# Optimization experiments

Measured on AMD Instinct MI355X. Metric: run time of the kernel, lower is better.

Reference implementation:

```python
import jax, jax.numpy as jnp
import numpy as np

D = 1024      # hidden_size
F = 4096      # intermediate_size
E = 16        # num_experts
TOPK = 2      # num_experts_per_tok
B, L = 1, 2048


def setup_inputs() -> dict:
    key = jax.random.key(0)
    ks = jax.random.split(key, 5)
    s = 0.02
    return {
        "x": jax.random.normal(ks[0], (B, L, D), dtype=jnp.float32),
        "gate_w": jax.random.normal(ks[1], (E, D), dtype=jnp.float32) * s,
        "w1s": jax.random.normal(ks[2], (E, F, D), dtype=jnp.float32) * s,  # per-expert w1 (out,in)
        "w2s": jax.random.normal(ks[3], (E, D, F), dtype=jnp.float32) * s,  # per-expert w2
        "w3s": jax.random.normal(ks[4], (E, F, D), dtype=jnp.float32) * s,  # per-expert w3
    }


def reference(x, gate_w, w1s, w2s, w3s):
    b, l, d = x.shape
    xf = x.reshape(-1, d)                                   # [T, D]
    router_logits = xf @ gate_w.T                           # [T, E]
    topw, topi = jax.lax.top_k(router_logits.astype(jnp.float32), TOPK)
    topw = jax.nn.softmax(topw, axis=-1).astype(x.dtype)    # [T, K]
    T = xf.shape[0]
    # dense combine weights: zero for unselected experts (same math as masked loop)
    combine = jnp.zeros((T, E), x.dtype).at[jnp.arange(T)[:, None], topi].add(topw)

    def body(acc, ew):
        w1, w2, w3, cw = ew                                 # cw: [T]
        h = jax.nn.silu(xf @ w1.T) * (xf @ w3.T)            # [T, F]
        return acc + cw[:, None] * (h @ w2.T), None

    out, _ = jax.lax.scan(body, jnp.zeros_like(xf), (w1s, w2s, w3s, combine.T))
    return out.reshape(b, l, d), router_logits
```

## Files before the change

kernel.cpp:

```cpp
#include <hip/hip_runtime.h>

#define D_DIM 1024
#define F_DIM 4096
#define E_NUM 16
#define T_NUM 2048

typedef __bf16 bf16x8 __attribute__((ext_vector_type(8)));
typedef float f32x4 __attribute__((ext_vector_type(4)));

__device__ __forceinline__ unsigned pack2bf(float a, float b) {
  unsigned ua = __builtin_bit_cast(unsigned, a);
  unsigned ub = __builtin_bit_cast(unsigned, b);
  return ((ub + 0x8000u) & 0xffff0000u) | ((ua + 0x8000u) >> 16);
}
__device__ __forceinline__ unsigned short f2bf(float a) {
  unsigned ua = __builtin_bit_cast(unsigned, a);
  return (unsigned short)((ua + 0x8000u) >> 16);
}
__device__ __forceinline__ bf16x8 cvt8(f32x4 a, f32x4 b) {
  bf16x8 r;
  r[0] = (__bf16)a[0]; r[1] = (__bf16)a[1]; r[2] = (__bf16)a[2]; r[3] = (__bf16)a[3];
  r[4] = (__bf16)b[0]; r[5] = (__bf16)b[1]; r[6] = (__bf16)b[2]; r[7] = (__bf16)b[3];
  return r;
}
__device__ __forceinline__ void gload16(const void* g, void* l) {
  __builtin_amdgcn_global_load_lds(
      (const __attribute__((address_space(1))) unsigned*)g,
      (__attribute__((address_space(3))) unsigned*)l, 16, 0, 0);
}

__global__ __launch_bounds__(256) void moe_xcast(
    const float* __restrict__ x, unsigned short* __restrict__ xbf)
{
  int i = blockIdx.x * 256 + threadIdx.x;
  const f32x4* p = (const f32x4*)x + (size_t)i * 2;
  f32x4 a = p[0], b = p[1];
  uint4 o;
  o.x = pack2bf(a[0], a[1]); o.y = pack2bf(a[2], a[3]);
  o.z = pack2bf(b[0], b[1]); o.w = pack2bf(b[2], b[3]);
  ((uint4*)xbf)[i] = o;
}

__global__ __launch_bounds__(256) void moe_router(
    const float* __restrict__ x, const float* __restrict__ gate,
    float* __restrict__ logits_out, int* __restrict__ topi, float* __restrict__ topw)
{
  __shared__ float lg[16][17];
  int tid = threadIdx.x;
  int tbase = blockIdx.x * 16;
  int tt = tid >> 4, e = tid & 15;
  const float4* xr = (const float4*)(x + (size_t)(tbase + tt) * D_DIM);
  const float4* gw = (const float4*)(gate + (size_t)e * D_DIM);
  float acc = 0.f;
  #pragma unroll 4
  for (int k = 0; k < D_DIM / 4; ++k) {
    float4 a = xr[k], b = gw[k];
    acc += a.x * b.x + a.y * b.y + a.z * b.z + a.w * b.w;
  }
  lg[tt][e] = acc;
  logits_out[(size_t)(tbase + tt) * E_NUM + e] = acc;
  __syncthreads();
  if (tid < 16) {
    int t = tid;
    float best = -1e30f; int i0 = 0;
    #pragma unroll
    for (int j = 0; j < 16; ++j) { float v = lg[t][j]; if (v > best) { best = v; i0 = j; } }
    float best1 = -1e30f; int i1 = 0;
    #pragma unroll
    for (int j = 0; j < 16; ++j) { if (j == i0) continue; float v = lg[t][j]; if (v > best1) { best1 = v; i1 = j; } }
    float e1 = __expf(best1 - best);
    float inv = 1.f / (1.f + e1);
    int gt = tbase + t;
    topi[gt * 2]     = i0;  topi[gt * 2 + 1] = i1;
    topw[gt * 2]     = inv; topw[gt * 2 + 1] = e1 * inv;
  }
}

__global__ __launch_bounds__(1024) void moe_route_build(
    const int* __restrict__ topi,
    int* __restrict__ cnt, int* __restrict__ rowbase,
    int* __restrict__ rowlist, int* __restrict__ rowpos)
{
  __shared__ int scnt[16];
  __shared__ int sbase[17];
  int wave = threadIdx.x >> 6;
  int lane = threadIdx.x & 63;
  int total = 0;
  for (int c = 0; c < (T_NUM * 2) / 64; ++c) {
    int s = c * 64 + lane;
    unsigned long long m = __ballot(topi[s] == wave);
    total += __popcll(m);
  }
  if (lane == 0) scnt[wave] = total;
  __syncthreads();
  if (threadIdx.x == 0) {
    int acc = 0;
    for (int e2 = 0; e2 < 16; ++e2) { sbase[e2] = acc; cnt[e2] = scnt[e2]; acc += scnt[e2]; }
    sbase[16] = acc;
    for (int e2 = 0; e2 <= 16; ++e2) rowbase[e2] = sbase[e2];
  }
  __syncthreads();
  int running = sbase[wave];
  for (int c = 0; c < (T_NUM * 2) / 64; ++c) {
    int s = c * 64 + lane;
    int ei = topi[s];
    unsigned long long m = __ballot(ei == wave);
    if (ei == wave) {
      int pos = running + __popcll(m & ((1ull << lane) - 1ull));
      rowlist[pos] = s;
      rowpos[s] = pos;
    }
    running += __popcll(m);
  }
}

__global__ __launch_bounds__(256, 2) void moe_gemm1(
    const unsigned short* __restrict__ xbf, const float* __restrict__ w1s, const float* __restrict__ w3s,
    const int* __restrict__ cnt, const int* __restrict__ rowbase, const int* __restrict__ rowlist,
    unsigned short* __restrict__ H)
{
  int e = blockIdx.z, mt = blockIdx.y, nt = blockIdx.x;
  int Ne = cnt[e];
  if (mt * 128 >= Ne) return;
  int rbase = rowbase[e];

  __shared__ char smem[81920];

  int tid = threadIdx.x, lane = tid & 63, wave = tid >> 6;

  const char* px[2];
  #pragma unroll
  for (int it = 0; it < 2; ++it) {
    int r = (wave * 2 + it) * 16 + (lane >> 2);
    int lr = mt * 128 + r;
    int tok = (lr < Ne) ? (rowlist[rbase + lr] >> 1) : 0;
    int c = (lane & 3) ^ ((r >> 1) & 3);
    px[it] = (const char*)(xbf + (size_t)tok * D_DIM) + c * 16;
  }
  const float* w1e = w1s + (size_t)e * F_DIM * D_DIM + (size_t)(nt * 128) * D_DIM;
  const float* w3e = w3s + (size_t)e * F_DIM * D_DIM + (size_t)(nt * 128) * D_DIM;
  const char* p1[4]; const char* p3[4];
  #pragma unroll
  for (int it = 0; it < 4; ++it) {
    int r = (wave * 4 + it) * 8 + (lane >> 3);
    int c = (lane & 7) ^ (r & 7);
    p1[it] = (const char*)(w1e + (size_t)r * D_DIM) + c * 16;
    p3[it] = (const char*)(w3e + (size_t)r * D_DIM) + c * 16;
  }

  int wm = wave >> 1, wn = wave & 1;
  int lr16 = lane & 15, lq = lane >> 4;

  unsigned offA[4];
  #pragma unroll
  for (int mi = 0; mi < 4; ++mi) {
    int m = wm * 64 + mi * 16 + lr16;
    offA[mi] = (unsigned)(m * 64 + ((lq ^ ((m >> 1) & 3)) * 16));
  }
  unsigned offB[4][2];
  #pragma unroll
  for (int ni = 0; ni < 4; ++ni) {
    int n = wn * 64 + ni * 16 + lr16;
    #pragma unroll
    for (int h = 0; h < 2; ++h)
      offB[ni][h] = (unsigned)(n * 128 + (((lq * 2 + h) ^ (n & 7)) * 16));
  }

  f32x4 acc1[4][4], acc3[4][4];
  #pragma unroll
  for (int i = 0; i < 4; ++i)
    #pragma unroll
    for (int j = 0; j < 4; ++j) { acc1[i][j] = {0.f,0.f,0.f,0.f}; acc3[i][j] = {0.f,0.f,0.f,0.f}; }

  unsigned xdst = (unsigned)((wave * 2) * 1024 + lane * 16);
  unsigned wdst = (unsigned)((wave * 4) * 1024 + lane * 16);

  auto STAGE = [&](unsigned bsel, int ks) {
    gload16(px[0] + ks * 64, smem + bsel * 8192 + xdst);
    gload16(px[1] + ks * 64, smem + bsel * 8192 + xdst + 1024);
    #pragma unroll
    for (int it = 0; it < 4; ++it) {
      gload16(p1[it] + ks * 128, smem + 16384 + bsel * 16384 + wdst + it * 1024);
      gload16(p3[it] + ks * 128, smem + 49152 + bsel * 16384 + wdst + it * 1024);
    }
  };

  STAGE(0, 0);
  unsigned buf = 0;
  for (int ks = 0; ks < 32; ++ks) {
    if (ks < 31) {
      STAGE(buf ^ 1u, ks + 1);
      asm volatile("s_waitcnt vmcnt(10)" ::: "memory");
    } else {
      asm volatile("s_waitcnt vmcnt(0)" ::: "memory");
    }
    __builtin_amdgcn_s_barrier();
    unsigned xb = buf * 8192;
    unsigned w1b = 16384 + buf * 16384;
    unsigned w3b = 49152 + buf * 16384;
    bf16x8 af[4], b1f[4], b3f[4];
    #pragma unroll
    for (int mi = 0; mi < 4; ++mi)
      af[mi] = *(const bf16x8*)(smem + xb + offA[mi]);
    #pragma unroll
    for (int ni = 0; ni < 4; ++ni) {
      b1f[ni] = cvt8(*(const f32x4*)(smem + w1b + offB[ni][0]),
                     *(const f32x4*)(smem + w1b + offB[ni][1]));
      b3f[ni] = cvt8(*(const f32x4*)(smem + w3b + offB[ni][0]),
                     *(const f32x4*)(smem + w3b + offB[ni][1]));
    }
    #pragma unroll
    for (int ni = 0; ni < 4; ++ni)
      #pragma unroll
      for (int mi = 0; mi < 4; ++mi) {
        acc1[mi][ni] = __builtin_amdgcn_mfma_f32_16x16x32_bf16(af[mi], b1f[ni], acc1[mi][ni], 0, 0, 0);
        acc3[mi][ni] = __builtin_amdgcn_mfma_f32_16x16x32_bf16(af[mi], b3f[ni], acc3[mi][ni], 0, 0, 0);
      }
    __builtin_amdgcn_s_barrier();
    buf ^= 1u;
  }

  #pragma unroll
  for (int mi = 0; mi < 4; ++mi) {
    int mb = wm * 64 + mi * 16 + lq * 4;
    #pragma unroll
    for (int r = 0; r < 4; ++r) {
      int lrow = mt * 128 + mb + r;
      if (lrow < Ne) {
        size_t hrow = (size_t)(rbase + lrow) * F_DIM;
        #pragma unroll
        for (int ni = 0; ni < 4; ++ni) {
          int f = nt * 128 + wn * 64 + ni * 16 + lr16;
          float a1v = acc1[mi][ni][r];
          float a3v = acc3[mi][ni][r];
          float hv = (a1v / (1.f + __expf(-a1v))) * a3v;
          H[hrow + f] = f2bf(hv);
        }
      }
    }
  }
}

__global__ __launch_bounds__(256, 2) void moe_gemm2(
    const unsigned short* __restrict__ H, const float* __restrict__ w2s,
    const int* __restrict__ cnt, const int* __restrict__ rowbase,
    unsigned short* __restrict__ Ybf)
{
  int e = blockIdx.z, mt = blockIdx.y, nt = blockIdx.x;
  int Ne = cnt[e];
  if (mt * 128 >= Ne) return;
  int rbase = rowbase[e];

  __shared__ char smem[65536];

  int tid = threadIdx.x, lane = tid & 63, wave = tid >> 6;

  const char* pa[4];
  #pragma unroll
  for (int it = 0; it < 4; ++it) {
    int r = (wave * 4 + it) * 8 + (lane >> 3);
    int c = (lane & 7) ^ (r & 7);
    int grow = mt * 128 + r; if (grow >= Ne) grow = Ne - 1;
    pa[it] = (const char*)(H + (size_t)(rbase + grow) * F_DIM) + c * 16;
  }
  const float* w2e = w2s + (size_t)e * D_DIM * F_DIM + (size_t)(nt * 64) * F_DIM;
  const char* pb[4];
  #pragma unroll
  for (int it = 0; it < 4; ++it) {
    int r = (wave * 4 + it) * 4 + (lane >> 4);
    int c = (lane & 15) ^ (r & 7);
    pb[it] = (const char*)(w2e + (size_t)r * F_DIM) + c * 16;
  }

  int wm = wave >> 1, wn = wave & 1;
  int lr16 = lane & 15, lq = lane >> 4;

  f32x4 acc[4][2];
  #pragma unroll
  for (int i = 0; i < 4; ++i) { acc[i][0] = {0.f,0.f,0.f,0.f}; acc[i][1] = {0.f,0.f,0.f,0.f}; }

  unsigned dst = (unsigned)((wave * 4) * 1024 + lane * 16);

  auto STAGE = [&](unsigned bsel, int ks) {
    #pragma unroll
    for (int it = 0; it < 4; ++it) {
      gload16(pa[it] + ks * 128, smem + bsel * 16384 + dst + it * 1024);
      gload16(pb[it] + ks * 256, smem + 32768 + bsel * 16384 + dst + it * 1024);
    }
  };

  STAGE(0, 0);
  unsigned buf = 0;
  for (int ks = 0; ks < 64; ++ks) {
    if (ks < 63) {
      STAGE(buf ^ 1u, ks + 1);
      asm volatile("s_waitcnt vmcnt(8)" ::: "memory");
    } else {
      asm volatile("s_waitcnt vmcnt(0)" ::: "memory");
    }
    __builtin_amdgcn_s_barrier();
    unsigned ab = buf * 16384;
    unsigned bb = 32768 + buf * 16384;
    #pragma unroll
    for (int ksub = 0; ksub < 2; ++ksub) {
      bf16x8 af[4], bf[2];
      #pragma unroll
      for (int mi = 0; mi < 4; ++mi) {
        int m = wm * 64 + mi * 16 + lr16;
        unsigned off = (unsigned)(m * 128 + (((ksub * 4 + lq) ^ (m & 7)) * 16));
        af[mi] = *(const bf16x8*)(smem + ab + off);
      }
      #pragma unroll
      for (int ni = 0; ni < 2; ++ni) {
        int n = wn * 32 + ni * 16 + lr16;
        unsigned o0 = (unsigned)(n * 256 + (((ksub * 8 + lq * 2 + 0) ^ (n & 7)) * 16));
        unsigned o1 = (unsigned)(n * 256 + (((ksub * 8 + lq * 2 + 1) ^ (n & 7)) * 16));
        bf[ni] = cvt8(*(const f32x4*)(smem + bb + o0), *(const f32x4*)(smem + bb + o1));
      }
      #pragma unroll
      for (int mi = 0; mi < 4; ++mi)
        #pragma unroll
        for (int ni = 0; ni < 2; ++ni)
          acc[mi][ni] = __builtin_amdgcn_mfma_f32_16x16x32_bf16(af[mi], bf[ni], acc[mi][ni], 0, 0, 0);
    }
    __builtin_amdgcn_s_barrier();
    buf ^= 1u;
  }

  #pragma unroll
  for (int mi = 0; mi < 4; ++mi) {
    int mb = wm * 64 + mi * 16 + lq * 4;
    #pragma unroll
    for (int r = 0; r < 4; ++r) {
      int lrow = mt * 128 + mb + r;
      if (lrow < Ne) {
        size_t yrow = (size_t)(rbase + lrow) * D_DIM;
        #pragma unroll
        for (int ni = 0; ni < 2; ++ni) {
          int d = nt * 64 + wn * 32 + ni * 16 + lr16;
          Ybf[yrow + d] = f2bf(acc[mi][ni][r]);
        }
      }
    }
  }
}

__global__ __launch_bounds__(128) void moe_combine(
    const unsigned short* __restrict__ Ybf, const int* __restrict__ rowpos,
    const float* __restrict__ topw, float* __restrict__ out)
{
  int t = blockIdx.x, tid = threadIdx.x;
  int r0 = rowpos[t * 2], r1 = rowpos[t * 2 + 1];
  float p0 = topw[t * 2], p1 = topw[t * 2 + 1];
  uint4 a = ((const uint4*)(Ybf + (size_t)r0 * D_DIM))[tid];
  uint4 b = ((const uint4*)(Ybf + (size_t)r1 * D_DIM))[tid];
  float4 o0, o1;
  #define LO(u) __builtin_bit_cast(float, (unsigned)((u) << 16))
  #define HI(u) __builtin_bit_cast(float, (unsigned)((u) & 0xffff0000u))
  o0.x = p0 * LO(a.x) + p1 * LO(b.x);  o0.y = p0 * HI(a.x) + p1 * HI(b.x);
  o0.z = p0 * LO(a.y) + p1 * LO(b.y);  o0.w = p0 * HI(a.y) + p1 * HI(b.y);
  o1.x = p0 * LO(a.z) + p1 * LO(b.z);  o1.y = p0 * HI(a.z) + p1 * HI(b.z);
  o1.z = p0 * LO(a.w) + p1 * LO(b.w);  o1.w = p0 * HI(a.w) + p1 * HI(b.w);
  #undef LO
  #undef HI
  float4* orow = (float4*)(out + (size_t)t * D_DIM);
  orow[tid * 2]     = o0;
  orow[tid * 2 + 1] = o1;
}

extern "C" void kernel_launch(void* const* d_in, const int* in_sizes, int n_in,
                              void* d_out, int out_size, void* d_ws, size_t ws_size,
                              hipStream_t stream) {
  const float* x    = (const float*)d_in[0];
  const float* gate = (const float*)d_in[1];
  const float* w1   = (const float*)d_in[2];
  const float* w2   = (const float*)d_in[3];
  const float* w3   = (const float*)d_in[4];
  float* out    = (float*)d_out;
  float* logits = out + (size_t)T_NUM * D_DIM;

  char* ws = (char*)d_ws;
  int*   cnt     = (int*)(ws + 0);
  int*   rowbase = (int*)(ws + 64);
  int*   topi    = (int*)(ws + 1024);
  float* topw    = (float*)(ws + 1024 + 16384);
  int*   rowlist = (int*)(ws + 1024 + 32768);
  int*   rowpos  = (int*)(ws + 1024 + 49152);
  unsigned short* H   = (unsigned short*)(ws + 131072);
  unsigned short* Ybf = (unsigned short*)(ws + 131072 + 33554432);
  unsigned short* xbf = (unsigned short*)(ws + 131072 + 33554432 + 8388608);

  moe_xcast<<<(T_NUM * D_DIM) / (256 * 8), 256, 0, stream>>>(x, xbf);
  moe_router<<<T_NUM / 16, 256, 0, stream>>>(x, gate, logits, topi, topw);
  moe_route_build<<<1, 1024, 0, stream>>>(topi, cnt, rowbase, rowlist, rowpos);
  moe_gemm1<<<dim3(F_DIM / 128, T_NUM / 128, E_NUM), 256, 0, stream>>>(xbf, w1, w3, cnt, rowbase, rowlist, H);
  moe_gemm2<<<dim3(D_DIM / 64, T_NUM / 128, E_NUM), 256, 0, stream>>>(H, w2, cnt, rowbase, Ybf);
  moe_combine<<<T_NUM, 128, 0, stream>>>(Ybf, rowpos, topw, out);
}
```

Measured before the change: 365.7 us.

## Use 8 waves per block in both MoE GEMMs, halving per-wave tile

Both expert GEMM kernels move from 256 to 512 threads per block. Each wave now computes a narrower N slice (2 subtiles in gemm1, 1 in gemm2), and the global-to-LDS staging work and vmcnt thresholds are split to match. The aim is more waves per CU to hide memory and LDS latency, at the cost of less register-level reuse of A fragments per wave and more LDS reads per MFMA. The launch bound of 4 blocks per CU may not be reachable given the 80KB/64KB LDS per block.

```diff
diff --git a/kernel.cpp b/kernel.cpp
--- a/kernel.cpp
+++ b/kernel.cpp
@@ -114,7 +114,7 @@
   }
 }
 
-__global__ __launch_bounds__(256, 2) void moe_gemm1(
+__global__ __launch_bounds__(512, 4) void moe_gemm1(
     const unsigned short* __restrict__ xbf, const float* __restrict__ w1s, const float* __restrict__ w3s,
     const int* __restrict__ cnt, const int* __restrict__ rowbase, const int* __restrict__ rowlist,
     unsigned short* __restrict__ H)
@@ -128,27 +128,26 @@
 
   int tid = threadIdx.x, lane = tid & 63, wave = tid >> 6;
 
-  const char* px[2];
-  #pragma unroll
-  for (int it = 0; it < 2; ++it) {
-    int r = (wave * 2 + it) * 16 + (lane >> 2);
-    int lr = mt * 128 + r;
-    int tok = (lr < Ne) ? (rowlist[rbase + lr] >> 1) : 0;
-    int c = (lane & 3) ^ ((r >> 1) & 3);
-    px[it] = (const char*)(xbf + (size_t)tok * D_DIM) + c * 16;
-  }
+  int xr = wave * 16 + (lane >> 2);
+  {
+  }
+  int xlr = mt * 128 + xr;
+  int xtok = (xlr < Ne) ? (rowlist[rbase + xlr] >> 1) : 0;
+  int xc = (lane & 3) ^ ((xr >> 1) & 3);
+  const char* px = (const char*)(xbf + (size_t)xtok * D_DIM) + xc * 16;
+
   const float* w1e = w1s + (size_t)e * F_DIM * D_DIM + (size_t)(nt * 128) * D_DIM;
   const float* w3e = w3s + (size_t)e * F_DIM * D_DIM + (size_t)(nt * 128) * D_DIM;
-  const char* p1[4]; const char* p3[4];
-  #pragma unroll
-  for (int it = 0; it < 4; ++it) {
-    int r = (wave * 4 + it) * 8 + (lane >> 3);
+  const char* p1[2]; const char* p3[2];
+  #pragma unroll
+  for (int it = 0; it < 2; ++it) {
+    int r = (wave * 2 + it) * 8 + (lane >> 3);
     int c = (lane & 7) ^ (r & 7);
     p1[it] = (const char*)(w1e + (size_t)r * D_DIM) + c * 16;
     p3[it] = (const char*)(w3e + (size_t)r * D_DIM) + c * 16;
   }
 
-  int wm = wave >> 1, wn = wave & 1;
+  int wm = wave >> 2, wn = wave & 3;
   int lr16 = lane & 15, lq = lane >> 4;
 
   unsigned offA[4];
@@ -157,29 +156,28 @@
     int m = wm * 64 + mi * 16 + lr16;
     offA[mi] = (unsigned)(m * 64 + ((lq ^ ((m >> 1) & 3)) * 16));
   }
-  unsigned offB[4][2];
-  #pragma unroll
-  for (int ni = 0; ni < 4; ++ni) {
-    int n = wn * 64 + ni * 16 + lr16;
+  unsigned offB[2][2];
+  #pragma unroll
+  for (int ni = 0; ni < 2; ++ni) {
+    int n = wn * 32 + ni * 16 + lr16;
     #pragma unroll
     for (int h = 0; h < 2; ++h)
       offB[ni][h] = (unsigned)(n * 128 + (((lq * 2 + h) ^ (n & 7)) * 16));
   }
 
-  f32x4 acc1[4][4], acc3[4][4];
+  f32x4 acc1[4][2], acc3[4][2];
   #pragma unroll
   for (int i = 0; i < 4; ++i)
     #pragma unroll
-    for (int j = 0; j < 4; ++j) { acc1[i][j] = {0.f,0.f,0.f,0.f}; acc3[i][j] = {0.f,0.f,0.f,0.f}; }
-
-  unsigned xdst = (unsigned)((wave * 2) * 1024 + lane * 16);
-  unsigned wdst = (unsigned)((wave * 4) * 1024 + lane * 16);
+    for (int j = 0; j < 2; ++j) { acc1[i][j] = {0.f,0.f,0.f,0.f}; acc3[i][j] = {0.f,0.f,0.f,0.f}; }
+
+  unsigned xdst = (unsigned)(wave * 1024 + lane * 16);
+  unsigned wdst = (unsigned)((wave * 2) * 1024 + lane * 16);
 
   auto STAGE = [&](unsigned bsel, int ks) {
-    gload16(px[0] + ks * 64, smem + bsel * 8192 + xdst);
-    gload16(px[1] + ks * 64, smem + bsel * 8192 + xdst + 1024);
-    #pragma unroll
-    for (int it = 0; it < 4; ++it) {
+    gload16(px + ks * 64, smem + bsel * 8192 + xdst);
+    #pragma unroll
+    for (int it = 0; it < 2; ++it) {
       gload16(p1[it] + ks * 128, smem + 16384 + bsel * 16384 + wdst + it * 1024);
       gload16(p3[it] + ks * 128, smem + 49152 + bsel * 16384 + wdst + it * 1024);
     }
@@ -190,7 +188,7 @@
   for (int ks = 0; ks < 32; ++ks) {
     if (ks < 31) {
       STAGE(buf ^ 1u, ks + 1);
-      asm volatile("s_waitcnt vmcnt(10)" ::: "memory");
+      asm volatile("s_waitcnt vmcnt(5)" ::: "memory");
     } else {
       asm volatile("s_waitcnt vmcnt(0)" ::: "memory");
     }
@@ -198,24 +196,22 @@
     unsigned xb = buf * 8192;
     unsigned w1b = 16384 + buf * 16384;
     unsigned w3b = 49152 + buf * 16384;
-    bf16x8 af[4], b1f[4], b3f[4];
+    bf16x8 af[4];
     #pragma unroll
     for (int mi = 0; mi < 4; ++mi)
       af[mi] = *(const bf16x8*)(smem + xb + offA[mi]);
     #pragma unroll
-    for (int ni = 0; ni < 4; ++ni) {
-      b1f[ni] = cvt8(*(const f32x4*)(smem + w1b + offB[ni][0]),
-                     *(const f32x4*)(smem + w1b + offB[ni][1]));
-      b3f[ni] = cvt8(*(const f32x4*)(smem + w3b + offB[ni][0]),
-                     *(const f32x4*)(smem + w3b + offB[ni][1]));
-    }
-    #pragma unroll
-    for (int ni = 0; ni < 4; ++ni)
+    for (int ni = 0; ni < 2; ++ni) {
+      bf16x8 b1 = cvt8(*(const f32x4*)(smem + w1b + offB[ni][0]),
+                       *(const f32x4*)(smem + w1b + offB[ni][1]));
+      bf16x8 b3 = cvt8(*(const f32x4*)(smem + w3b + offB[ni][0]),
+                       *(const f32x4*)(smem + w3b + offB[ni][1]));
       #pragma unroll
       for (int mi = 0; mi < 4; ++mi) {
-        acc1[mi][ni] = __builtin_amdgcn_mfma_f32_16x16x32_bf16(af[mi], b1f[ni], acc1[mi][ni], 0, 0, 0);
-        acc3[mi][ni] = __builtin_amdgcn_mfma_f32_16x16x32_bf16(af[mi], b3f[ni], acc3[mi][ni], 0, 0, 0);
-      }
+        acc1[mi][ni] = __builtin_amdgcn_mfma_f32_16x16x32_bf16(af[mi], b1, acc1[mi][ni], 0, 0, 0);
+        acc3[mi][ni] = __builtin_amdgcn_mfma_f32_16x16x32_bf16(af[mi], b3, acc3[mi][ni], 0, 0, 0);
+      }
+    }
     __builtin_amdgcn_s_barrier();
     buf ^= 1u;
   }
@@ -229,8 +225,8 @@
       if (lrow < Ne) {
         size_t hrow = (size_t)(rbase + lrow) * F_DIM;
         #pragma unroll
-        for (int ni = 0; ni < 4; ++ni) {
-          int f = nt * 128 + wn * 64 + ni * 16 + lr16;
+        for (int ni = 0; ni < 2; ++ni) {
+          int f = nt * 128 + wn * 32 + ni * 16 + lr16;
           float a1v = acc1[mi][ni][r];
           float a3v = acc3[mi][ni][r];
           float hv = (a1v / (1.f + __expf(-a1v))) * a3v;
@@ -241,7 +237,7 @@
   }
 }
 
-__global__ __launch_bounds__(256, 2) void moe_gemm2(
+__global__ __launch_bounds__(512, 4) void moe_gemm2(
     const unsigned short* __restrict__ H, const float* __restrict__ w2s,
     const int* __restrict__ cnt, const int* __restrict__ rowbase,
     unsigned short* __restrict__ Ybf)
@@ -255,35 +251,35 @@
 
   int tid = threadIdx.x, lane = tid & 63, wave = tid >> 6;
 
-  const char* pa[4];
-  #pragma unroll
-  for (int it = 0; it < 4; ++it) {
-    int r = (wave * 4 + it) * 8 + (lane >> 3);
+  const char* pa[2];
+  #pragma unroll
+  for (int it = 0; it < 2; ++it) {
+    int r = (wave * 2 + it) * 8 + (lane >> 3);
     int c = (lane & 7) ^ (r & 7);
     int grow = mt * 128 + r; if (grow >= Ne) grow = Ne - 1;
     pa[it] = (const char*)(H + (size_t)(rbase + grow) * F_DIM) + c * 16;
   }
   const float* w2e = w2s + (size_t)e * D_DIM * F_DIM + (size_t)(nt * 64) * F_DIM;
-  const char* pb[4];
-  #pragma unroll
-  for (int it = 0; it < 4; ++it) {
-    int r = (wave * 4 + it) * 4 + (lane >> 4);
+  const char* pb[2];
+  #pragma unroll
+  for (int it = 0; it < 2; ++it) {
+    int r = (wave * 2 + it) * 4 + (lane >> 4);
     int c = (lane & 15) ^ (r & 7);
     pb[it] = (const char*)(w2e + (size_t)r * F_DIM) + c * 16;
   }
 
-  int wm = wave >> 1, wn = wave & 1;
+  int wm = wave >> 2, wn = wave & 3;
   int lr16 = lane & 15, lq = lane >> 4;
 
-  f32x4 acc[4][2];
-  #pragma unroll
-  for (int i = 0; i < 4; ++i) { acc[i][0] = {0.f,0.f,0.f,0.f}; acc[i][1] = {0.f,0.f,0.f,0.f}; }
-
-  unsigned dst = (unsigned)((wave * 4) * 1024 + lane * 16);
+  f32x4 acc[4];
+  #pragma unroll
+  for (int i = 0; i < 4; ++i) acc[i] = {0.f,0.f,0.f,0.f};
+
+  unsigned dst = (unsigned)((wave * 2) * 1024 + lane * 16);
 
   auto STAGE = [&](unsigned bsel, int ks) {
     #pragma unroll
-    for (int it = 0; it < 4; ++it) {
+    for (int it = 0; it < 2; ++it) {
       gload16(pa[it] + ks * 128, smem + bsel * 16384 + dst + it * 1024);
       gload16(pb[it] + ks * 256, smem + 32768 + bsel * 16384 + dst + it * 1024);
     }
@@ -294,34 +290,29 @@
   for (int ks = 0; ks < 64; ++ks) {
     if (ks < 63) {
       STAGE(buf ^ 1u, ks + 1);
-      asm volatile("s_waitcnt vmcnt(8)" ::: "memory");
+      asm volatile("s_waitcnt vmcnt(4)" ::: "memory");
     } else {
       asm volatile("s_waitcnt vmcnt(0)" ::: "memory");
     }
     __builtin_amdgcn_s_barrier();
     unsigned ab = buf * 16384;
     unsigned bb = 32768 + buf * 16384;
+    int n = wn * 16 + lr16;
     #pragma unroll
     for (int ksub = 0; ksub < 2; ++ksub) {
-      bf16x8 af[4], bf[2];
+      bf16x8 bf;
+      {
+        unsigned o0 = (unsigned)(n * 256 + (((ksub * 8 + lq * 2 + 0) ^ (n & 7)) * 16));
+        unsigned o1 = (unsigned)(n * 256 + (((ksub * 8 + lq * 2 + 1) ^ (n & 7)) * 16));
+        bf = cvt8(*(const f32x4*)(smem + bb + o0), *(const f32x4*)(smem + bb + o1));
+      }
       #pragma unroll
       for (int mi = 0; mi < 4; ++mi) {
         int m = wm * 64 + mi * 16 + lr16;
         unsigned off = (unsigned)(m * 128 + (((ksub * 4 + lq) ^ (m & 7)) * 16));
-        af[mi] = *(const bf16x8*)(smem + ab + off);
-      }
-      #pragma unroll
-      for (int ni = 0; ni < 2; ++ni) {
-        int n = wn * 32 + ni * 16 + lr16;
-        unsigned o0 = (unsigned)(n * 256 + (((ksub * 8 + lq * 2 + 0) ^ (n & 7)) * 16));
-        unsigned o1 = (unsigned)(n * 256 + (((ksub * 8 + lq * 2 + 1) ^ (n & 7)) * 16));
-        bf[ni] = cvt8(*(const f32x4*)(smem + bb + o0), *(const f32x4*)(smem + bb + o1));
-      }
-      #pragma unroll
-      for (int mi = 0; mi < 4; ++mi)
-        #pragma unroll
-        for (int ni = 0; ni < 2; ++ni)
-          acc[mi][ni] = __builtin_amdgcn_mfma_f32_16x16x32_bf16(af[mi], bf[ni], acc[mi][ni], 0, 0, 0);
+        bf16x8 af = *(const bf16x8*)(smem + ab + off);
+        acc[mi] = __builtin_amdgcn_mfma_f32_16x16x32_bf16(af, bf, acc[mi], 0, 0, 0);
+      }
     }
     __builtin_amdgcn_s_barrier();
     buf ^= 1u;
@@ -335,11 +326,8 @@
       int lrow = mt * 128 + mb + r;
       if (lrow < Ne) {
         size_t yrow = (size_t)(rbase + lrow) * D_DIM;
-        #pragma unroll
-        for (int ni = 0; ni < 2; ++ni) {
-          int d = nt * 64 + wn * 32 + ni * 16 + lr16;
-          Ybf[yrow + d] = f2bf(acc[mi][ni][r]);
-        }
+        int d = nt * 64 + wn * 16 + lr16;
+        Ybf[yrow + d] = f2bf(acc[mi][r]);
       }
     }
   }
@@ -393,7 +381,7 @@
   moe_xcast<<<(T_NUM * D_DIM) / (256 * 8), 256, 0, stream>>>(x, xbf);
   moe_router<<<T_NUM / 16, 256, 0, stream>>>(x, gate, logits, topi, topw);
   moe_route_build<<<1, 1024, 0, stream>>>(topi, cnt, rowbase, rowlist, rowpos);
-  moe_gemm1<<<dim3(F_DIM / 128, T_NUM / 128, E_NUM), 256, 0, stream>>>(xbf, w1, w3, cnt, rowbase, rowlist, H);
-  moe_gemm2<<<dim3(D_DIM / 64, T_NUM / 128, E_NUM), 256, 0, stream>>>(H, w2, cnt, rowbase, Ybf);
+  moe_gemm1<<<dim3(F_DIM / 128, T_NUM / 128, E_NUM), 512, 0, stream>>>(xbf, w1, w3, cnt, rowbase, rowlist, H);
+  moe_gemm2<<<dim3(D_DIM / 64, T_NUM / 128, E_NUM), 512, 0, stream>>>(H, w2, cnt, rowbase, Ybf);
   moe_combine<<<T_NUM, 128, 0, stream>>>(Ybf, rowpos, topw, out);
 }
```

After: 370.2 us. No clear change (+1.2%).

## Make MoE GEMMs persistent per expert/N-tile with 256-row tiles and XCD mapping

Applied to the files above, without the earlier changes.

Both expert GEMMs now launch one 512-thread block per (expert, N-tile) and loop over 256-row M tiles inside the block, instead of launching a 3D grid of 128-row tiles. Block IDs are mapped so that each expert's blocks land on the same XCD, which should let the fp32 weight tiles be shared in that XCD's L2. Doubling the M tile to 256 rows cuts how many times the large fp32 weights are streamed from memory, since a typical expert now fits in one tile. The cost is possible load imbalance across experts with different token counts, and fewer independent blocks to hide latency.

```diff
diff --git a/kernel.cpp b/kernel.cpp
--- a/kernel.cpp
+++ b/kernel.cpp
@@ -114,40 +114,41 @@
   }
 }
 
-__global__ __launch_bounds__(256, 2) void moe_gemm1(
+__global__ __launch_bounds__(512, 2) void moe_gemm1(
     const unsigned short* __restrict__ xbf, const float* __restrict__ w1s, const float* __restrict__ w3s,
     const int* __restrict__ cnt, const int* __restrict__ rowbase, const int* __restrict__ rowlist,
     unsigned short* __restrict__ H)
 {
-  int e = blockIdx.z, mt = blockIdx.y, nt = blockIdx.x;
+  int bid = blockIdx.x;
+  int xcd = bid & 7, j = bid >> 3;
+  int e = xcd * 2 + (j >> 5);
+  int nt = j & 31;
   int Ne = cnt[e];
-  if (mt * 128 >= Ne) return;
   int rbase = rowbase[e];
-
-  __shared__ char smem[81920];
+  int nmt = (Ne + 255) >> 8;
+
+  __shared__ char smem[98304];
 
   int tid = threadIdx.x, lane = tid & 63, wave = tid >> 6;
 
-  const char* px[2];
-  #pragma unroll
-  for (int it = 0; it < 2; ++it) {
-    int r = (wave * 2 + it) * 16 + (lane >> 2);
-    int lr = mt * 128 + r;
-    int tok = (lr < Ne) ? (rowlist[rbase + lr] >> 1) : 0;
-    int c = (lane & 3) ^ ((r >> 1) & 3);
-    px[it] = (const char*)(xbf + (size_t)tok * D_DIM) + c * 16;
-  }
   const float* w1e = w1s + (size_t)e * F_DIM * D_DIM + (size_t)(nt * 128) * D_DIM;
   const float* w3e = w3s + (size_t)e * F_DIM * D_DIM + (size_t)(nt * 128) * D_DIM;
-  const char* p1[4]; const char* p3[4];
-  #pragma unroll
-  for (int it = 0; it < 4; ++it) {
-    int r = (wave * 4 + it) * 8 + (lane >> 3);
+  const char* p1[2]; const char* p3[2];
+  #pragma unroll
+  for (int it = 0; it < 2; ++it) {
+    int r = (wave * 2 + it) * 8 + (lane >> 3);
     int c = (lane & 7) ^ (r & 7);
     p1[it] = (const char*)(w1e + (size_t)r * D_DIM) + c * 16;
     p3[it] = (const char*)(w3e + (size_t)r * D_DIM) + c * 16;
   }
 
+  int xrr[2]; int xc[2];
+  #pragma unroll
+  for (int it = 0; it < 2; ++it) {
+    xrr[it] = (wave * 2 + it) * 16 + (lane >> 2);
+    xc[it] = (lane & 3) ^ ((xrr[it] >> 1) & 3);
+  }
+
   int wm = wave >> 1, wn = wave & 1;
   int lr16 = lane & 15, lq = lane >> 4;
 
@@ -166,179 +167,198 @@
       offB[ni][h] = (unsigned)(n * 128 + (((lq * 2 + h) ^ (n & 7)) * 16));
   }
 
-  f32x4 acc1[4][4], acc3[4][4];
-  #pragma unroll
-  for (int i = 0; i < 4; ++i)
-    #pragma unroll
-    for (int j = 0; j < 4; ++j) { acc1[i][j] = {0.f,0.f,0.f,0.f}; acc3[i][j] = {0.f,0.f,0.f,0.f}; }
-
   unsigned xdst = (unsigned)((wave * 2) * 1024 + lane * 16);
-  unsigned wdst = (unsigned)((wave * 4) * 1024 + lane * 16);
-
-  auto STAGE = [&](unsigned bsel, int ks) {
-    gload16(px[0] + ks * 64, smem + bsel * 8192 + xdst);
-    gload16(px[1] + ks * 64, smem + bsel * 8192 + xdst + 1024);
-    #pragma unroll
-    for (int it = 0; it < 4; ++it) {
-      gload16(p1[it] + ks * 128, smem + 16384 + bsel * 16384 + wdst + it * 1024);
-      gload16(p3[it] + ks * 128, smem + 49152 + bsel * 16384 + wdst + it * 1024);
-    }
-  };
-
-  STAGE(0, 0);
-  unsigned buf = 0;
-  for (int ks = 0; ks < 32; ++ks) {
-    if (ks < 31) {
-      STAGE(buf ^ 1u, ks + 1);
-      asm volatile("s_waitcnt vmcnt(10)" ::: "memory");
-    } else {
-      asm volatile("s_waitcnt vmcnt(0)" ::: "memory");
-    }
-    __builtin_amdgcn_s_barrier();
-    unsigned xb = buf * 8192;
-    unsigned w1b = 16384 + buf * 16384;
-    unsigned w3b = 49152 + buf * 16384;
-    bf16x8 af[4], b1f[4], b3f[4];
-    #pragma unroll
-    for (int mi = 0; mi < 4; ++mi)
-      af[mi] = *(const bf16x8*)(smem + xb + offA[mi]);
-    #pragma unroll
-    for (int ni = 0; ni < 4; ++ni) {
-      b1f[ni] = cvt8(*(const f32x4*)(smem + w1b + offB[ni][0]),
-                     *(const f32x4*)(smem + w1b + offB[ni][1]));
-      b3f[ni] = cvt8(*(const f32x4*)(smem + w3b + offB[ni][0]),
-                     *(const f32x4*)(smem + w3b + offB[ni][1]));
-    }
-    #pragma unroll
-    for (int ni = 0; ni < 4; ++ni)
-      #pragma unroll
-      for (int mi = 0; mi < 4; ++mi) {
-        acc1[mi][ni] = __builtin_amdgcn_mfma_f32_16x16x32_bf16(af[mi], b1f[ni], acc1[mi][ni], 0, 0, 0);
-        acc3[mi][ni] = __builtin_amdgcn_mfma_f32_16x16x32_bf16(af[mi], b3f[ni], acc3[mi][ni], 0, 0, 0);
-      }
-    __builtin_amdgcn_s_barrier();
-    buf ^= 1u;
-  }
-
-  #pragma unroll
-  for (int mi = 0; mi < 4; ++mi) {
-    int mb = wm * 64 + mi * 16 + lq * 4;
-    #pragma unroll
-    for (int r = 0; r < 4; ++r) {
-      int lrow = mt * 128 + mb + r;
-      if (lrow < Ne) {
-        size_t hrow = (size_t)(rbase + lrow) * F_DIM;
+  unsigned wdst = (unsigned)((wave * 2) * 1024 + lane * 16);
+
+  for (int mt = 0; mt < nmt; ++mt) {
+    const char* px[2];
+    #pragma unroll
+    for (int it = 0; it < 2; ++it) {
+      int xlr = mt * 256 + xrr[it];
+      int tok = (xlr < Ne) ? (rowlist[rbase + xlr] >> 1) : 0;
+      px[it] = (const char*)(xbf + (size_t)tok * D_DIM) + xc[it] * 16;
+    }
+
+    f32x4 acc1[4][4], acc3[4][4];
+    #pragma unroll
+    for (int i = 0; i < 4; ++i)
+      #pragma unroll
+      for (int jj = 0; jj < 4; ++jj) { acc1[i][jj] = {0.f,0.f,0.f,0.f}; acc3[i][jj] = {0.f,0.f,0.f,0.f}; }
+
+    auto STAGE = [&](unsigned bsel, int ks) {
+      gload16(px[0] + ks * 64, smem + bsel * 16384 + xdst);
+      gload16(px[1] + ks * 64, smem + bsel * 16384 + xdst + 1024);
+      #pragma unroll
+      for (int it = 0; it < 2; ++it) {
+        gload16(p1[it] + ks * 128, smem + 32768 + bsel * 16384 + wdst + it * 1024);
+        gload16(p3[it] + ks * 128, smem + 65536 + bsel * 16384 + wdst + it * 1024);
+      }
+    };
+
+    STAGE(0, 0);
+    unsigned buf = 0;
+    for (int ks = 0; ks < 32; ++ks) {
+      if (ks < 31) {
+        STAGE(buf ^ 1u, ks + 1);
+        asm volatile("s_waitcnt vmcnt(6)" ::: "memory");
+      } else {
+        asm volatile("s_waitcnt vmcnt(0)" ::: "memory");
+      }
+      __builtin_amdgcn_s_barrier();
+      unsigned xb = buf * 16384;
+      unsigned w1b = 32768 + buf * 16384;
+      unsigned w3b = 65536 + buf * 16384;
+      bf16x8 af[4];
+      #pragma unroll
+      for (int mi = 0; mi < 4; ++mi)
+        af[mi] = *(const bf16x8*)(smem + xb + offA[mi]);
+      #pragma unroll
+      for (int ni = 0; ni < 4; ++ni) {
+        bf16x8 b1 = cvt8(*(const f32x4*)(smem + w1b + offB[ni][0]),
+                         *(const f32x4*)(smem + w1b + offB[ni][1]));
+        bf16x8 b3 = cvt8(*(const f32x4*)(smem + w3b + offB[ni][0]),
+                         *(const f32x4*)(smem + w3b + offB[ni][1]));
         #pragma unroll
-        for (int ni = 0; ni < 4; ++ni) {
-          int f = nt * 128 + wn * 64 + ni * 16 + lr16;
-          float a1v = acc1[mi][ni][r];
-          float a3v = acc3[mi][ni][r];
-          float hv = (a1v / (1.f + __expf(-a1v))) * a3v;
-          H[hrow + f] = f2bf(hv);
+        for (int mi = 0; mi < 4; ++mi) {
+          acc1[mi][ni] = __builtin_amdgcn_mfma_f32_16x16x32_bf16(af[mi], b1, acc1[mi][ni], 0, 0, 0);
+          acc3[mi][ni] = __builtin_amdgcn_mfma_f32_16x16x32_bf16(af[mi], b3, acc3[mi][ni], 0, 0, 0);
         }
       }
-    }
-  }
-}
-
-__global__ __launch_bounds__(256, 2) void moe_gemm2(
+      __builtin_amdgcn_s_barrier();
+      buf ^= 1u;
+    }
+
+    #pragma unroll
+    for (int mi = 0; mi < 4; ++mi) {
+      int mb = wm * 64 + mi * 16 + lq * 4;
+      #pragma unroll
+      for (int r = 0; r < 4; ++r) {
+        int lrow = mt * 256 + mb + r;
+        if (lrow < Ne) {
+          size_t hrow = (size_t)(rbase + lrow) * F_DIM;
+          #pragma unroll
+          for (int ni = 0; ni < 4; ++ni) {
+            int f = nt * 128 + wn * 64 + ni * 16 + lr16;
+            float a1v = acc1[mi][ni][r];
+            float a3v = acc3[mi][ni][r];
+            float hv = (a1v / (1.f + __expf(-a1v))) * a3v;
+            H[hrow + f] = f2bf(hv);
+          }
+        }
+      }
+    }
+  }
+}
+
+__global__ __launch_bounds__(512, 2) void moe_gemm2(
     const unsigned short* __restrict__ H, const float* __restrict__ w2s,
     const int* __restrict__ cnt, const int* __restrict__ rowbase,
     unsigned short* __restrict__ Ybf)
 {
-  int e = blockIdx.z, mt = blockIdx.y, nt = blockIdx.x;
+  int bid = blockIdx.x;
+  int xcd = bid & 7, j = bid >> 3;
+  int e = xcd * 2 + (j >> 4);
+  int nt = j & 15;
   int Ne = cnt[e];
-  if (mt * 128 >= Ne) return;
   int rbase = rowbase[e];
-
-  __shared__ char smem[65536];
+  int nmt = (Ne + 255) >> 8;
+
+  __shared__ char smem[98304];
 
   int tid = threadIdx.x, lane = tid & 63, wave = tid >> 6;
 
-  const char* pa[4];
-  #pragma unroll
-  for (int it = 0; it < 4; ++it) {
-    int r = (wave * 4 + it) * 8 + (lane >> 3);
-    int c = (lane & 7) ^ (r & 7);
-    int grow = mt * 128 + r; if (grow >= Ne) grow = Ne - 1;
-    pa[it] = (const char*)(H + (size_t)(rbase + grow) * F_DIM) + c * 16;
-  }
   const float* w2e = w2s + (size_t)e * D_DIM * F_DIM + (size_t)(nt * 64) * F_DIM;
-  const char* pb[4];
-  #pragma unroll
-  for (int it = 0; it < 4; ++it) {
-    int r = (wave * 4 + it) * 4 + (lane >> 4);
+  const char* pb[2];
+  #pragma unroll
+  for (int it = 0; it < 2; ++it) {
+    int r = (wave * 2 + it) * 4 + (lane >> 4);
     int c = (lane & 15) ^ (r & 7);
     pb[it] = (const char*)(w2e + (size_t)r * F_DIM) + c * 16;
   }
 
+  int arr[4]; int ac[4];
+  #pragma unroll
+  for (int it = 0; it < 4; ++it) {
+    arr[it] = (wave * 4 + it) * 8 + (lane >> 3);
+    ac[it] = (lane & 7) ^ (arr[it] & 7);
+  }
+
   int wm = wave >> 1, wn = wave & 1;
   int lr16 = lane & 15, lq = lane >> 4;
 
-  f32x4 acc[4][2];
-  #pragma unroll
-  for (int i = 0; i < 4; ++i) { acc[i][0] = {0.f,0.f,0.f,0.f}; acc[i][1] = {0.f,0.f,0.f,0.f}; }
-
-  unsigned dst = (unsigned)((wave * 4) * 1024 + lane * 16);
-
-  auto STAGE = [&](unsigned bsel, int ks) {
+  unsigned dst2 = (unsigned)((wave * 2) * 1024 + lane * 16);
+  unsigned dst4 = (unsigned)((wave * 4) * 1024 + lane * 16);
+
+  for (int mt = 0; mt < nmt; ++mt) {
+    const char* pa[4];
     #pragma unroll
     for (int it = 0; it < 4; ++it) {
-      gload16(pa[it] + ks * 128, smem + bsel * 16384 + dst + it * 1024);
-      gload16(pb[it] + ks * 256, smem + 32768 + bsel * 16384 + dst + it * 1024);
-    }
-  };
-
-  STAGE(0, 0);
-  unsigned buf = 0;
-  for (int ks = 0; ks < 64; ++ks) {
-    if (ks < 63) {
-      STAGE(buf ^ 1u, ks + 1);
-      asm volatile("s_waitcnt vmcnt(8)" ::: "memory");
-    } else {
-      asm volatile("s_waitcnt vmcnt(0)" ::: "memory");
-    }
-    __builtin_amdgcn_s_barrier();
-    unsigned ab = buf * 16384;
-    unsigned bb = 32768 + buf * 16384;
-    #pragma unroll
-    for (int ksub = 0; ksub < 2; ++ksub) {
-      bf16x8 af[4], bf[2];
-      #pragma unroll
-      for (int mi = 0; mi < 4; ++mi) {
-        int m = wm * 64 + mi * 16 + lr16;
-        unsigned off = (unsigned)(m * 128 + (((ksub * 4 + lq) ^ (m & 7)) * 16));
-        af[mi] = *(const bf16x8*)(smem + ab + off);
-      }
-      #pragma unroll
-      for (int ni = 0; ni < 2; ++ni) {
-        int n = wn * 32 + ni * 16 + lr16;
-        unsigned o0 = (unsigned)(n * 256 + (((ksub * 8 + lq * 2 + 0) ^ (n & 7)) * 16));
-        unsigned o1 = (unsigned)(n * 256 + (((ksub * 8 + lq * 2 + 1) ^ (n & 7)) * 16));
-        bf[ni] = cvt8(*(const f32x4*)(smem + bb + o0), *(const f32x4*)(smem + bb + o1));
-      }
-      #pragma unroll
-      for (int mi = 0; mi < 4; ++mi)
-        #pragma unroll
-        for (int ni = 0; ni < 2; ++ni)
-          acc[mi][ni] = __builtin_amdgcn_mfma_f32_16x16x32_bf16(af[mi], bf[ni], acc[mi][ni], 0, 0, 0);
-    }
-    __builtin_amdgcn_s_barrier();
-    buf ^= 1u;
-  }
-
-  #pragma unroll
-  for (int mi = 0; mi < 4; ++mi) {
-    int mb = wm * 64 + mi * 16 + lq * 4;
-    #pragma unroll
-    for (int r = 0; r < 4; ++r) {
-      int lrow = mt * 128 + mb + r;
-      if (lrow < Ne) {
-        size_t yrow = (size_t)(rbase + lrow) * D_DIM;
+      int grow = mt * 256 + arr[it]; if (grow >= Ne) grow = Ne - 1;
+      pa[it] = (const char*)(H + (size_t)(rbase + grow) * F_DIM) + ac[it] * 16;
+    }
+
+    f32x4 acc[4][2];
+    #pragma unroll
+    for (int i = 0; i < 4; ++i) { acc[i][0] = {0.f,0.f,0.f,0.f}; acc[i][1] = {0.f,0.f,0.f,0.f}; }
+
+    auto STAGE = [&](unsigned bsel, int ks) {
+      #pragma unroll
+      for (int it = 0; it < 4; ++it)
+        gload16(pa[it] + ks * 128, smem + bsel * 32768 + dst4 + it * 1024);
+      #pragma unroll
+      for (int it = 0; it < 2; ++it)
+        gload16(pb[it] + ks * 256, smem + 65536 + bsel * 16384 + dst2 + it * 1024);
+    };
+
+    STAGE(0, 0);
+    unsigned buf = 0;
+    for (int ks = 0; ks < 64; ++ks) {
+      if (ks < 63) {
+        STAGE(buf ^ 1u, ks + 1);
+        asm volatile("s_waitcnt vmcnt(6)" ::: "memory");
+      } else {
+        asm volatile("s_waitcnt vmcnt(0)" ::: "memory");
+      }
+      __builtin_amdgcn_s_barrier();
+      unsigned ab = buf * 32768;
+      unsigned bb = 65536 + buf * 16384;
+      #pragma unroll
+      for (int ksub = 0; ksub < 2; ++ksub) {
+        bf16x8 bfr[2];
         #pragma unroll
         for (int ni = 0; ni < 2; ++ni) {
-          int d = nt * 64 + wn * 32 + ni * 16 + lr16;
-          Ybf[yrow + d] = f2bf(acc[mi][ni][r]);
+          int n = wn * 32 + ni * 16 + lr16;
+          unsigned o0 = (unsigned)(n * 256 + (((ksub * 8 + lq * 2 + 0) ^ (n & 7)) * 16));
+          unsigned o1 = (unsigned)(n * 256 + (((ksub * 8 + lq * 2 + 1) ^ (n & 7)) * 16));
+          bfr[ni] = cvt8(*(const f32x4*)(smem + bb + o0), *(const f32x4*)(smem + bb + o1));
+        }
+        #pragma unroll
+        for (int mi = 0; mi < 4; ++mi) {
+          int m = wm * 64 + mi * 16 + lr16;
+          unsigned off = (unsigned)(m * 128 + (((ksub * 4 + lq) ^ (m & 7)) * 16));
+          bf16x8 af = *(const bf16x8*)(smem + ab + off);
+          #pragma unroll
+          for (int ni = 0; ni < 2; ++ni)
+            acc[mi][ni] = __builtin_amdgcn_mfma_f32_16x16x32_bf16(af, bfr[ni], acc[mi][ni], 0, 0, 0);
+        }
+      }
+      __builtin_amdgcn_s_barrier();
+      buf ^= 1u;
+    }
+
+    #pragma unroll
+    for (int mi = 0; mi < 4; ++mi) {
+      int mb = wm * 64 + mi * 16 + lq * 4;
+      #pragma unroll
+      for (int r = 0; r < 4; ++r) {
+        int lrow = mt * 256 + mb + r;
+        if (lrow < Ne) {
+          size_t yrow = (size_t)(rbase + lrow) * D_DIM;
+          #pragma unroll
+          for (int ni = 0; ni < 2; ++ni) {
+            int d = nt * 64 + wn * 32 + ni * 16 + lr16;
+            Ybf[yrow + d] = f2bf(acc[mi][ni][r]);
+          }
         }
       }
     }
@@ -393,7 +413,7 @@
   moe_xcast<<<(T_NUM * D_DIM) / (256 * 8), 256, 0, stream>>>(x, xbf);
   moe_router<<<T_NUM / 16, 256, 0, stream>>>(x, gate, logits, topi, topw);
   moe_route_build<<<1, 1024, 0, stream>>>(topi, cnt, rowbase, rowlist, rowpos);
-  moe_gemm1<<<dim3(F_DIM / 128, T_NUM / 128, E_NUM), 256, 0, stream>>>(xbf, w1, w3, cnt, rowbase, rowlist, H);
-  moe_gemm2<<<dim3(D_DIM / 64, T_NUM / 128, E_NUM), 256, 0, stream>>>(H, w2, cnt, rowbase, Ybf);
+  moe_gemm1<<<512, 512, 0, stream>>>(xbf, w1, w3, cnt, rowbase, rowlist, H);
+  moe_gemm2<<<256, 512, 0, stream>>>(H, w2, cnt, rowbase, Ybf);
   moe_combine<<<T_NUM, 128, 0, stream>>>(Ybf, rowpos, topw, out);
 }
```

New measurement: 381.4 us. 1.04x slower.
